# Kernel optimization log

Measured on AMD Instinct MI355X. Metric: run time of the kernel, lower is better.

## Reference

```python
import jax, jax.numpy as jnp
import numpy as np

B, C, N, H = 2, 512, 3072, 8
D = C // H  # head_dim = 64


def setup_inputs() -> dict:
    key = jax.random.key(0)
    ks = jax.random.split(key, 8)
    s = 1.0 / np.sqrt(C)
    x = jax.random.normal(ks[0], (B, C, N), dtype=jnp.float32)
    adj = jax.random.randint(ks[1], (N, N), 0, 2, dtype=jnp.int32)
    adj = adj.at[jnp.arange(N), jnp.arange(N)].set(1)  # self-loops avoid empty rows
    geo_bias = jax.random.normal(ks[2], (N, N), dtype=jnp.float32) * 0.02
    Wq = jax.random.normal(ks[3], (C, C), dtype=jnp.float32) * s
    Wk = jax.random.normal(ks[4], (C, C), dtype=jnp.float32) * s
    Wv = jax.random.normal(ks[5], (C, C), dtype=jnp.float32) * s
    Wo = jax.random.normal(ks[6], (C, C), dtype=jnp.float32) * s
    z = jnp.zeros((C,), dtype=jnp.float32)
    return {"x": x, "adjacency": adj, "geo_bias": geo_bias,
            "Wq": Wq, "bq": z, "Wk": Wk, "bk": z, "Wv": Wv, "bv": z,
            "Wo": Wo, "bo": z}


def reference(x, adjacency, geo_bias, Wq, bq, Wk, bk, Wv, bv, Wo, bo):
    b, c, n = x.shape
    h, d = H, c // H
    feats = jnp.swapaxes(x, 1, 2)  # [B, N, C]
    # projections (nn.Linear: y = x @ W^T + b)
    q = feats @ Wq.T + bq
    k = feats @ Wk.T + bk
    v = feats @ Wv.T + bv
    # [B, H, N, D]
    q = q.reshape(b, n, h, d).transpose(0, 2, 1, 3)
    k = k.reshape(b, n, h, d).transpose(0, 2, 1, 3)
    v = v.reshape(b, n, h, d).transpose(0, 2, 1, 3)
    scores = jnp.einsum('bhnd,bhmd->bhnm', q, k) / jnp.sqrt(jnp.float32(d))
    scores = scores + geo_bias[None, None]
    scores = jnp.where(adjacency[None, None] == 0, -jnp.inf, scores)
    weights = jax.nn.softmax(scores, axis=-1)
    attended = jnp.einsum('bhnm,bhmd->bhnd', weights, v)
    attended = attended.transpose(0, 2, 1, 3).reshape(b, n, c)
    out = attended @ Wo.T + bo
    return jnp.swapaxes(out, 1, 2)  # [B, C, N]
```

## Files before the change

kernel.cpp:

```cpp
#include <hip/hip_runtime.h>

constexpr int Bb = 2, Cc = 512, Nn = 3072, Hh = 8, Dd = 64;
constexpr int BN = Bb * Nn;
constexpr int NT = Nn / 64;
constexpr int NTI = Nn / 128;

typedef __bf16 bf16;
typedef __attribute__((ext_vector_type(8))) __bf16 bf16x8;
typedef __attribute__((ext_vector_type(4))) __bf16 bf16x4;
typedef __attribute__((ext_vector_type(4))) float f32x4;
typedef __attribute__((ext_vector_type(16))) float f32x16;
typedef unsigned int u32;
typedef __attribute__((ext_vector_type(4))) u32 u32x4;

#define DEVINL static __device__ __forceinline__

DEVINL bf16x8 ldb8(const bf16* p) { return *reinterpret_cast<const bf16x8*>(p); }

DEVINL void gload_lds16(const bf16* g, bf16* l) {
    __builtin_amdgcn_global_load_lds(
        (const __attribute__((address_space(1))) void*)g,
        (__attribute__((address_space(3))) void*)l, 16, 0, 0);
}

DEVINL u32 cvtpk(float lo, float hi) {
    u32 r;
    asm("v_cvt_pk_bf16_f32 %0, %1, %2" : "=v"(r) : "v"(lo), "v"(hi));
    return r;
}
DEVINL void plswap(u32& a, u32& b) {
    asm("v_permlane32_swap_b32 %0, %1" : "+v"(a), "+v"(b));
}
DEVINL float xpair_sum(float v) { return v + __shfl_xor(v, 32); }

__global__ void k_tx(const float* __restrict__ x, bf16* __restrict__ feats) {
    __shared__ float t[32][33];
    const int b = blockIdx.z;
    const int n0 = blockIdx.x * 32, c0 = blockIdx.y * 32;
    const int tx = threadIdx.x, ty = threadIdx.y;
#pragma unroll
    for (int i = 0; i < 4; ++i)
        t[ty + i * 8][tx] = x[((size_t)b * Cc + c0 + ty + i * 8) * Nn + n0 + tx];
    __syncthreads();
#pragma unroll
    for (int i = 0; i < 4; ++i)
        feats[((size_t)b * Nn + n0 + ty + i * 8) * Cc + c0 + tx] = (bf16)t[tx][ty + i * 8];
}

__global__ void k_packw(const float* __restrict__ Wq, const float* __restrict__ Wk,
                        const float* __restrict__ Wv, const float* __restrict__ Wo,
                        bf16* __restrict__ Wqkv, bf16* __restrict__ WoB) {
    const int i = blockIdx.x * 256 + threadIdx.x;
    Wqkv[i]              = (bf16)Wq[i];
    Wqkv[i + 262144]     = (bf16)Wk[i];
    Wqkv[i + 524288]     = (bf16)Wv[i];
    WoB[i]               = (bf16)Wo[i];
}

__global__ void k_biasm(const int* __restrict__ adj, const float* __restrict__ gb,
                        bf16* __restrict__ biasF) {
    const int ti = blockIdx.x, tj = blockIdx.y;
    bf16* outp = biasF + ((size_t)ti * NT + tj) * 8192;
#pragma unroll
    for (int it = 0; it < 32; ++it) {
        const int p = it * 256 + threadIdx.x;
        const int w = p >> 11, hi = (p >> 10) & 1, l31 = (p >> 5) & 31;
        const int kt2 = (p >> 4) & 1, reg = p & 15;
        const int row = w * 32 + l31;
        const int col = kt2 * 32 + (reg & 3) + 8 * (reg >> 2) + 4 * hi;
        const size_t src = (size_t)(ti * 128 + row) * Nn + tj * 64 + col;
        outp[p] = adj[src] ? (bf16)(gb[src] * 1.44269504f) : (bf16)(-1e30f);
    }
}

#define STAGEG(dst, srcbase, ldk, k0, bi)                                      \
    {                                                                          \
        _Pragma("unroll")                                                      \
        for (int ps = 0; ps < 2; ++ps) {                                       \
            const int s = ps * 256 + tid;                                      \
            const int pr = s >> 3, pcb = s & 7;                                \
            const int cb = pcb ^ (pr & 7);                                     \
            gload_lds16((srcbase) + (size_t)pr * (ldk) + (k0) + cb * 8,        \
                        &dst[bi][(ps * 4 + w) * 512]);                         \
        }                                                                      \
    }

__global__ __launch_bounds__(256) void k_qkv(
        const bf16* __restrict__ feats, const bf16* __restrict__ Wqkv,
        const float* __restrict__ bq, const float* __restrict__ bk, const float* __restrict__ bv,
        bf16* __restrict__ Q, bf16* __restrict__ K, bf16* __restrict__ Vt) {
    __shared__ bf16 sA[2][4096];
    __shared__ bf16 sB[2][4096];
    const int m0 = blockIdx.x * 64;
    const int n0 = blockIdx.y * 64;
    const int tid = threadIdx.x, w = tid >> 6, lane = tid & 63;
    const int lg = lane >> 4, lc = lane & 15;

    f32x4 acc[4];
    const f32x4 z4 = {0.f, 0.f, 0.f, 0.f};
#pragma unroll
    for (int jt = 0; jt < 4; ++jt) acc[jt] = z4;

    const bf16* Abase = feats + (size_t)m0 * Cc;
    const bf16* Bbase = Wqkv + (size_t)n0 * Cc;

    int buf = 0;
    STAGEG(sA, Abase, Cc, 0, 0);
    STAGEG(sB, Bbase, Cc, 0, 0);
    for (int kk = 0; kk < 8; ++kk) {
        const int kn = (kk + 1 < 8) ? kk + 1 : 7;
        STAGEG(sA, Abase, Cc, kn * 64, buf ^ 1);
        STAGEG(sB, Bbase, Cc, kn * 64, buf ^ 1);
        asm volatile("s_waitcnt vmcnt(4)" ::: "memory");
        __builtin_amdgcn_s_barrier();
        const int ra = w * 16 + lc;
#pragma unroll
        for (int ks = 0; ks < 2; ++ks) {
            bf16x8 a = ldb8(&sA[buf][ra * 64 + (((ks * 4 + lg) ^ (ra & 7)) * 8)]);
#pragma unroll
            for (int jt = 0; jt < 4; ++jt) {
                const int rb = jt * 16 + lc;
                bf16x8 bfr = ldb8(&sB[buf][rb * 64 + (((ks * 4 + lg) ^ (rb & 7)) * 8)]);
                acc[jt] = __builtin_amdgcn_mfma_f32_16x16x32_bf16(a, bfr, acc[jt], 0, 0, 0);
            }
        }
        __builtin_amdgcn_s_barrier();
        buf ^= 1;
    }
    asm volatile("s_waitcnt vmcnt(0)" ::: "memory");

    const int proj = n0 >> 9;
    const int head = (n0 >> 6) & 7;
    const float* bias = proj == 0 ? bq : (proj == 1 ? bk : bv);
#pragma unroll
    for (int jt = 0; jt < 4; ++jt) {
        const int dcol = jt * 16 + lc;
        const float bs = bias[(n0 & 511) + dcol];
#pragma unroll
        for (int r = 0; r < 4; ++r) {
            const int m = m0 + w * 16 + lg * 4 + r;
            const int b = m / Nn;
            const int n = m - b * Nn;
            const float v = acc[jt][r] + bs;
            if (proj == 0)
                Q[(((size_t)b * Hh + head) * Nn + n) * Dd + dcol] = (bf16)v;
            else if (proj == 1)
                K[(((size_t)b * Hh + head) * Nn + n) * Dd + dcol] = (bf16)v;
            else
                Vt[(((size_t)b * Hh + head) * Dd + dcol) * Nn + n] = (bf16)v;
        }
    }
}

template <bool DIRECT, int TCNT>
__global__ __launch_bounds__(256) void k_attn(
        const bf16* __restrict__ Q, const bf16* __restrict__ K, const bf16* __restrict__ Vt,
        const bf16* __restrict__ biasF, bf16* __restrict__ att,
        float* __restrict__ pO, float* __restrict__ pL) {
    __shared__ bf16 sK[2][4096];
    __shared__ bf16 sV[2][4096];

    const int ti = blockIdx.x;
    const int i0 = ti * 128;
    const int bh = blockIdx.y;
    const int b = bh >> 3, h = bh & 7;
    const int sp = blockIdx.z;
    const int t0 = sp * TCNT;
    const int tid = threadIdx.x, w = tid >> 6, lane = tid & 63;
    const int l31 = lane & 31, hi = lane >> 5;

    const bf16* Qb = Q  + (size_t)bh * Nn * Dd;
    const bf16* Kb = K  + (size_t)bh * Nn * Dd;
    const bf16* Vb = Vt + (size_t)bh * Dd * Nn;
    const bf16* bp = biasF + (size_t)ti * NT * 8192 + (size_t)(w * 64 + lane) * 32;

    bf16x8 aq[4];
    {
        const bf16* qp = Qb + (size_t)(i0 + w * 32 + l31) * Dd + hi * 8;
#pragma unroll
        for (int dm = 0; dm < 4; ++dm) aq[dm] = ldb8(qp + dm * 16);
    }

    f32x16 acc[2];
#pragma unroll
    for (int dm = 0; dm < 2; ++dm)
#pragma unroll
        for (int i = 0; i < 16; ++i) acc[dm][i] = 0.f;
    float l16[16];
#pragma unroll
    for (int i = 0; i < 16; ++i) l16[i] = 0.f;

    constexpr float cqk = 0.18033688011112042f;

#define STAGE(bi, j0)                                                          \
    {                                                                          \
        _Pragma("unroll")                                                      \
        for (int u = 0; u < 2; ++u) {                                          \
            const int s = u * 256 + tid;                                       \
            const int pr = s >> 3, pcb = s & 7;                                \
            const int cb = pcb ^ (pr & 7);                                     \
            gload_lds16(Kb + (size_t)((j0) + pr) * Dd + cb * 8,                \
                        &sK[bi][(u * 4 + w) * 512]);                           \
            gload_lds16(Vb + (size_t)pr * Nn + (j0) + cb * 8,                  \
                        &sV[bi][(u * 4 + w) * 512]);                           \
        }                                                                      \
    }

    int buf = 0;
    STAGE(0, t0 * 64);
    bf16x8 bcur[4];
#pragma unroll
    for (int f = 0; f < 4; ++f) bcur[f] = ldb8(bp + (size_t)t0 * 8192 + f * 8);

    for (int u0 = 0; u0 < TCNT; ++u0) {
        const int tj = t0 + u0;
        const int tjn = (u0 + 1 < TCNT) ? tj + 1 : tj;
        STAGE(buf ^ 1, tjn * 64);
        bf16x8 bnx[4];
#pragma unroll
        for (int f = 0; f < 4; ++f) bnx[f] = ldb8(bp + (size_t)tjn * 8192 + f * 8);

        asm volatile("s_waitcnt vmcnt(8)" ::: "memory");
        __builtin_amdgcn_s_barrier();

        f32x16 s0, s1;
#pragma unroll
        for (int i = 0; i < 16; ++i) { s0[i] = 0.f; s1[i] = 0.f; }
#pragma unroll
        for (int dm = 0; dm < 4; ++dm) {
            const int r0 = l31;
            bf16x8 kf0 = ldb8(&sK[buf][r0 * 64 + (((dm * 2 + hi) ^ (r0 & 7)) * 8)]);
            s0 = __builtin_amdgcn_mfma_f32_32x32x16_bf16(kf0, aq[dm], s0, 0, 0, 0);
            const int r1 = 32 + l31;
            bf16x8 kf1 = ldb8(&sK[buf][r1 * 64 + (((dm * 2 + hi) ^ (r1 & 7)) * 8)]);
            s1 = __builtin_amdgcn_mfma_f32_32x32x16_bf16(kf1, aq[dm], s1, 0, 0, 0);
        }

        float sv[32];
#pragma unroll
        for (int i = 0; i < 16; ++i)
            sv[i] = __builtin_amdgcn_exp2f(__builtin_fmaf(s0[i], cqk, (float)bcur[i >> 3][i & 7]));
#pragma unroll
        for (int i = 0; i < 16; ++i)
            sv[16 + i] = __builtin_amdgcn_exp2f(__builtin_fmaf(s1[i], cqk, (float)bcur[2 + (i >> 3)][i & 7]));

#pragma unroll
        for (int i = 0; i < 16; ++i) l16[i] += sv[i] + sv[i + 16];

        bf16x8 pf[4];
#pragma unroll
        for (int g = 0; g < 4; ++g) {
            u32 X0 = cvtpk(sv[g * 8 + 0], sv[g * 8 + 1]);
            u32 X1 = cvtpk(sv[g * 8 + 2], sv[g * 8 + 3]);
            u32 Y0 = cvtpk(sv[g * 8 + 4], sv[g * 8 + 5]);
            u32 Y1 = cvtpk(sv[g * 8 + 6], sv[g * 8 + 7]);
            plswap(X0, Y0);
            plswap(X1, Y1);
            u32x4 t4 = {X0, X1, Y0, Y1};
            pf[g] = __builtin_bit_cast(bf16x8, t4);
        }

#pragma unroll
        for (int dm = 0; dm < 2; ++dm)
#pragma unroll
            for (int kt = 0; kt < 4; ++kt) {
                const int rv = dm * 32 + l31;
                bf16x8 vf = ldb8(&sV[buf][rv * 64 + (((kt * 2 + hi) ^ (rv & 7)) * 8)]);
                acc[dm] = __builtin_amdgcn_mfma_f32_32x32x16_bf16(vf, pf[kt], acc[dm], 0, 0, 0);
            }

        __builtin_amdgcn_s_barrier();
#pragma unroll
        for (int f = 0; f < 4; ++f) bcur[f] = bnx[f];
        buf ^= 1;
    }
    asm volatile("s_waitcnt vmcnt(0)" ::: "memory");

#pragma unroll
    for (int i = 0; i < 8; ++i) l16[i] += l16[i + 8];
#pragma unroll
    for (int i = 0; i < 4; ++i) l16[i] += l16[i + 4];
    float lrow = (l16[0] + l16[1]) + (l16[2] + l16[3]);
    lrow = xpair_sum(lrow);

    const int q = i0 + w * 32 + l31;
    if (DIRECT) {
        const float inv = 1.f / lrow;
        bf16* ap = att + ((size_t)b * Nn + q) * Cc + h * 64;
#pragma unroll
        for (int dm = 0; dm < 2; ++dm)
#pragma unroll
            for (int rg = 0; rg < 4; ++rg) {
                bf16x4 o;
#pragma unroll
                for (int i = 0; i < 4; ++i) o[i] = (bf16)(acc[dm][rg * 4 + i] * inv);
                *reinterpret_cast<bf16x4*>(ap + dm * 32 + rg * 8 + hi * 4) = o;
            }
    } else {
        float* op = pO + ((size_t)(sp * Bb * Hh + bh) * Nn + q) * Dd;
#pragma unroll
        for (int dm = 0; dm < 2; ++dm)
#pragma unroll
            for (int rg = 0; rg < 4; ++rg) {
                f32x4 o;
#pragma unroll
                for (int i = 0; i < 4; ++i) o[i] = acc[dm][rg * 4 + i];
                *reinterpret_cast<f32x4*>(op + dm * 32 + rg * 8 + hi * 4) = o;
            }
        if (hi == 0) pL[(size_t)(sp * Bb * Hh + bh) * Nn + q] = lrow;
    }
#undef STAGE
}

__global__ __launch_bounds__(256) void k_comb(const float* __restrict__ pO,
                                              const float* __restrict__ pL,
                                              bf16* __restrict__ att, int nsplit) {
    const int bh = blockIdx.y, b = bh >> 3, h = bh & 7;
    const int q = blockIdx.x * 64 + (threadIdx.x >> 2);
    const int d0 = (threadIdx.x & 3) * 16;
    const size_t base = ((size_t)bh * Nn + q) * Dd + d0;
    const size_t soff = (size_t)Bb * Hh * Nn * Dd;
    float l = pL[(size_t)bh * Nn + q];
    f32x4 o[4];
#pragma unroll
    for (int i = 0; i < 4; ++i) o[i] = *reinterpret_cast<const f32x4*>(pO + base + i * 4);
    if (nsplit == 2) {
        l += pL[(size_t)Bb * Hh * Nn + (size_t)bh * Nn + q];
#pragma unroll
        for (int i = 0; i < 4; ++i) {
            f32x4 o2 = *reinterpret_cast<const f32x4*>(pO + soff + base + i * 4);
#pragma unroll
            for (int j = 0; j < 4; ++j) o[i][j] += o2[j];
        }
    }
    const float inv = 1.f / l;
    bf16* ap = att + ((size_t)b * Nn + q) * Cc + h * 64 + d0;
#pragma unroll
    for (int i = 0; i < 4; ++i) {
        bf16x4 ov;
#pragma unroll
        for (int j = 0; j < 4; ++j) ov[j] = (bf16)(o[i][j] * inv);
        *reinterpret_cast<bf16x4*>(ap + i * 4) = ov;
    }
}

__global__ __launch_bounds__(256) void k_out(
        const bf16* __restrict__ att, const bf16* __restrict__ WoB,
        const float* __restrict__ bo, float* __restrict__ out) {
    __shared__ bf16 sA[2][4096];
    __shared__ bf16 sB[2][4096];
    const int m0 = blockIdx.x * 64;
    const int n0 = blockIdx.y * 64;
    const int tid = threadIdx.x, w = tid >> 6, lane = tid & 63;
    const int lg = lane >> 4, lc = lane & 15;

    f32x4 acc[4];
    const f32x4 z4 = {0.f, 0.f, 0.f, 0.f};
#pragma unroll
    for (int jt = 0; jt < 4; ++jt) acc[jt] = z4;

    const bf16* Abase = att + (size_t)m0 * Cc;
    const bf16* Bbase = WoB + (size_t)n0 * Cc;

    int buf = 0;
    STAGEG(sA, Abase, Cc, 0, 0);
    STAGEG(sB, Bbase, Cc, 0, 0);
    for (int kk = 0; kk < 8; ++kk) {
        const int kn = (kk + 1 < 8) ? kk + 1 : 7;
        STAGEG(sA, Abase, Cc, kn * 64, buf ^ 1);
        STAGEG(sB, Bbase, Cc, kn * 64, buf ^ 1);
        asm volatile("s_waitcnt vmcnt(4)" ::: "memory");
        __builtin_amdgcn_s_barrier();
        const int ra = w * 16 + lc;
#pragma unroll
        for (int ks = 0; ks < 2; ++ks) {
            bf16x8 a = ldb8(&sA[buf][ra * 64 + (((ks * 4 + lg) ^ (ra & 7)) * 8)]);
#pragma unroll
            for (int jt = 0; jt < 4; ++jt) {
                const int rb = jt * 16 + lc;
                bf16x8 bfr = ldb8(&sB[buf][rb * 64 + (((ks * 4 + lg) ^ (rb & 7)) * 8)]);
                acc[jt] = __builtin_amdgcn_mfma_f32_16x16x32_bf16(a, bfr, acc[jt], 0, 0, 0);
            }
        }
        __builtin_amdgcn_s_barrier();
        buf ^= 1;
    }
    asm volatile("s_waitcnt vmcnt(0)" ::: "memory");

    const int m = m0 + w * 16 + lg * 4;
    const int b = m / Nn;
    const int n = m - b * Nn;
#pragma unroll
    for (int jt = 0; jt < 4; ++jt) {
        const int col = n0 + jt * 16 + lc;
        const float bs = bo[col];
        f32x4 vv;
#pragma unroll
        for (int r = 0; r < 4; ++r) vv[r] = acc[jt][r] + bs;
        *reinterpret_cast<f32x4*>(&out[((size_t)b * Cc + col) * Nn + n]) = vv;
    }
}

extern "C" void kernel_launch(void* const* d_in, const int* in_sizes, int n_in,
                              void* d_out, int out_size, void* d_ws, size_t ws_size,
                              hipStream_t stream) {
    (void)in_sizes; (void)n_in; (void)out_size;
    const float* x  = (const float*)d_in[0];
    const int*   adj= (const int*)d_in[1];
    const float* gb = (const float*)d_in[2];
    const float* Wq = (const float*)d_in[3];
    const float* bq = (const float*)d_in[4];
    const float* Wk = (const float*)d_in[5];
    const float* bk = (const float*)d_in[6];
    const float* Wv = (const float*)d_in[7];
    const float* bv = (const float*)d_in[8];
    const float* Wo = (const float*)d_in[9];
    const float* bo = (const float*)d_in[10];
    float* out = (float*)d_out;

    char* ws = (char*)d_ws;
    bf16*  feats = (bf16*)(ws);
    bf16*  Wqkv  = (bf16*)(ws + 6291456);
    bf16*  WoB   = (bf16*)(ws + 7864320);
    bf16*  Qm    = (bf16*)(ws + 8388608);
    bf16*  Km    = (bf16*)(ws + 14680064);
    bf16*  Vt    = (bf16*)(ws + 20971520);
    bf16*  att   = (bf16*)(ws + 27262976);
    bf16*  biasF = (bf16*)(ws + 33554432);
    float* pO    = (float*)(ws + 52428800);
    float* pL    = (float*)(ws + 52428800 + 2 * 12582912);
    float* pL1   = (float*)(ws + 52428800 + 12582912);

    const size_t need2 = 52428800ull + 2 * 12582912ull + 2 * 196608ull;
    const size_t need1 = 52428800ull + 12582912ull + 196608ull;

    k_tx   <<<dim3(Nn / 32, Cc / 32, Bb), dim3(32, 8), 0, stream>>>(x, feats);
    k_packw<<<dim3(1024), dim3(256), 0, stream>>>(Wq, Wk, Wv, Wo, Wqkv, WoB);
    k_biasm<<<dim3(NTI, NT), dim3(256), 0, stream>>>(adj, gb, biasF);
    k_qkv  <<<dim3(BN / 64, 1536 / 64), dim3(256), 0, stream>>>(feats, Wqkv, bq, bk, bv, Qm, Km, Vt);

    if (ws_size >= need2) {
        k_attn<false, NT / 2><<<dim3(NTI, Bb * Hh, 2), dim3(256), 0, stream>>>(
            Qm, Km, Vt, biasF, att, pO, pL);
        k_comb<<<dim3(Nn / 64, Bb * Hh), dim3(256), 0, stream>>>(pO, pL, att, 2);
    } else if (ws_size >= need1) {
        k_attn<false, NT><<<dim3(NTI, Bb * Hh, 1), dim3(256), 0, stream>>>(
            Qm, Km, Vt, biasF, att, pO, pL1);
        k_comb<<<dim3(Nn / 64, Bb * Hh), dim3(256), 0, stream>>>(pO, pL1, att, 1);
    } else {
        k_attn<true, NT><<<dim3(NTI, Bb * Hh, 1), dim3(256), 0, stream>>>(
            Qm, Km, Vt, biasF, att, pO, pL);
    }
    k_out  <<<dim3(BN / 64, Cc / 64), dim3(256), 0, stream>>>(att, WoB, bo, out);
}
```

Measured before the change: 150.6 us.

## Split attention KV range four ways and raise wave priority around MFMA blocks

Adds a 4-way split of the key range in the attention kernel when the workspace is large enough, launching 4x the blocks along z, and generalizes the combine kernel to sum an arbitrary number of partial outputs and row sums. It also wraps the QK and PV MFMA loops in s_setprio raise/lower so waves issuing matrix work get scheduling priority over waves doing the exp/convert phase. The split aims to fill the GPU with more workgroups (the 2-way grid is only 24x16x2 blocks), at the cost of writing and re-reading more fp32 partial results in the combine step.

```diff
diff --git a/kernel.cpp b/kernel.cpp
--- a/kernel.cpp
+++ b/kernel.cpp
@@ -226,6 +226,7 @@
         f32x16 s0, s1;
 #pragma unroll
         for (int i = 0; i < 16; ++i) { s0[i] = 0.f; s1[i] = 0.f; }
+        __builtin_amdgcn_s_setprio(1);
 #pragma unroll
         for (int dm = 0; dm < 4; ++dm) {
             const int r0 = l31;
@@ -235,6 +236,7 @@
             bf16x8 kf1 = ldb8(&sK[buf][r1 * 64 + (((dm * 2 + hi) ^ (r1 & 7)) * 8)]);
             s1 = __builtin_amdgcn_mfma_f32_32x32x16_bf16(kf1, aq[dm], s1, 0, 0, 0);
         }
+        __builtin_amdgcn_s_setprio(0);
 
         float sv[32];
 #pragma unroll
@@ -260,6 +262,7 @@
             pf[g] = __builtin_bit_cast(bf16x8, t4);
         }
 
+        __builtin_amdgcn_s_setprio(1);
 #pragma unroll
         for (int dm = 0; dm < 2; ++dm)
 #pragma unroll
@@ -268,6 +271,7 @@
                 bf16x8 vf = ldb8(&sV[buf][rv * 64 + (((kt * 2 + hi) ^ (rv & 7)) * 8)]);
                 acc[dm] = __builtin_amdgcn_mfma_f32_32x32x16_bf16(vf, pf[kt], acc[dm], 0, 0, 0);
             }
+        __builtin_amdgcn_s_setprio(0);
 
         __builtin_amdgcn_s_barrier();
 #pragma unroll
@@ -320,15 +324,16 @@
     const int d0 = (threadIdx.x & 3) * 16;
     const size_t base = ((size_t)bh * Nn + q) * Dd + d0;
     const size_t soff = (size_t)Bb * Hh * Nn * Dd;
-    float l = pL[(size_t)bh * Nn + q];
+    const size_t loff = (size_t)Bb * Hh * Nn;
+    float l = 0.f;
     f32x4 o[4];
 #pragma unroll
-    for (int i = 0; i < 4; ++i) o[i] = *reinterpret_cast<const f32x4*>(pO + base + i * 4);
-    if (nsplit == 2) {
-        l += pL[(size_t)Bb * Hh * Nn + (size_t)bh * Nn + q];
+    for (int i = 0; i < 4; ++i) o[i] = f32x4{0.f, 0.f, 0.f, 0.f};
+    for (int s = 0; s < nsplit; ++s) {
+        l += pL[s * loff + (size_t)bh * Nn + q];
 #pragma unroll
         for (int i = 0; i < 4; ++i) {
-            f32x4 o2 = *reinterpret_cast<const f32x4*>(pO + soff + base + i * 4);
+            f32x4 o2 = *reinterpret_cast<const f32x4*>(pO + s * soff + base + i * 4);
 #pragma unroll
             for (int j = 0; j < 4; ++j) o[i][j] += o2[j];
         }
@@ -428,28 +433,35 @@
     bf16*  att   = (bf16*)(ws + 27262976);
     bf16*  biasF = (bf16*)(ws + 33554432);
     float* pO    = (float*)(ws + 52428800);
-    float* pL    = (float*)(ws + 52428800 + 2 * 12582912);
-    float* pL1   = (float*)(ws + 52428800 + 12582912);
-
-    const size_t need2 = 52428800ull + 2 * 12582912ull + 2 * 196608ull;
-    const size_t need1 = 52428800ull + 12582912ull + 196608ull;
+
+    const size_t PO1 = 12582912ull, PL1 = 196608ull, BASE = 52428800ull;
+    const size_t need4 = BASE + 4 * PO1 + 4 * PL1;
+    const size_t need2 = BASE + 2 * PO1 + 2 * PL1;
+    const size_t need1 = BASE + 1 * PO1 + 1 * PL1;
 
     k_tx   <<<dim3(Nn / 32, Cc / 32, Bb), dim3(32, 8), 0, stream>>>(x, feats);
     k_packw<<<dim3(1024), dim3(256), 0, stream>>>(Wq, Wk, Wv, Wo, Wqkv, WoB);
     k_biasm<<<dim3(NTI, NT), dim3(256), 0, stream>>>(adj, gb, biasF);
     k_qkv  <<<dim3(BN / 64, 1536 / 64), dim3(256), 0, stream>>>(feats, Wqkv, bq, bk, bv, Qm, Km, Vt);
 
-    if (ws_size >= need2) {
+    if (ws_size >= need4) {
+        float* pL = (float*)(ws + BASE + 4 * PO1);
+        k_attn<false, NT / 4><<<dim3(NTI, Bb * Hh, 4), dim3(256), 0, stream>>>(
+            Qm, Km, Vt, biasF, att, pO, pL);
+        k_comb<<<dim3(Nn / 64, Bb * Hh), dim3(256), 0, stream>>>(pO, pL, att, 4);
+    } else if (ws_size >= need2) {
+        float* pL = (float*)(ws + BASE + 2 * PO1);
         k_attn<false, NT / 2><<<dim3(NTI, Bb * Hh, 2), dim3(256), 0, stream>>>(
             Qm, Km, Vt, biasF, att, pO, pL);
         k_comb<<<dim3(Nn / 64, Bb * Hh), dim3(256), 0, stream>>>(pO, pL, att, 2);
     } else if (ws_size >= need1) {
+        float* pL = (float*)(ws + BASE + 1 * PO1);
         k_attn<false, NT><<<dim3(NTI, Bb * Hh, 1), dim3(256), 0, stream>>>(
-            Qm, Km, Vt, biasF, att, pO, pL1);
-        k_comb<<<dim3(Nn / 64, Bb * Hh), dim3(256), 0, stream>>>(pO, pL1, att, 1);
+            Qm, Km, Vt, biasF, att, pO, pL);
+        k_comb<<<dim3(Nn / 64, Bb * Hh), dim3(256), 0, stream>>>(pO, pL, att, 1);
     } else {
         k_attn<true, NT><<<dim3(NTI, Bb * Hh, 1), dim3(256), 0, stream>>>(
-            Qm, Km, Vt, biasF, att, pO, pL);
+            Qm, Km, Vt, biasF, att, pO, (float*)pO);
     }
     k_out  <<<dim3(BN / 64, Cc / 64), dim3(256), 0, stream>>>(att, WoB, bo, out);
 }
```

After: 156.9 us. +4.2%, slower.
